# Optimization experiments

Measured on AMD Instinct MI355X. Metric: run time of the kernel, lower is better.

The kernel has to match this reference:

```python
import jax, jax.numpy as jnp
import numpy as np

D, K, RANK = 128, 64, 16

def setup_inputs() -> dict:
    key = jax.random.key(0)
    k1, k2, k3, k4, k5 = jax.random.split(key, 5)
    x1 = jax.random.normal(k1, (8, 16384, D), dtype=jnp.float32)
    x2 = jax.random.normal(k2, (8, 16384, D), dtype=jnp.float32)
    scale = (RANK * D) ** -0.5
    W_lin = jax.random.normal(k3, (K, D), dtype=jnp.float32) * (D ** -0.5)
    P = jax.random.normal(k4, (K, D, RANK), dtype=jnp.float32) * scale
    Q = jax.random.normal(k5, (K, D, RANK), dtype=jnp.float32) * scale
    return {"x1": x1, "x2": x2, "W_lin": W_lin, "P": P, "Q": Q}

def reference(x1, x2, W_lin, P, Q):
    z = x1 - x2                                   # (b,n,d)
    s = x1 + x2                                   # (b,n,d)
    lin = jnp.einsum('bnd,kd->bnk', z, W_lin)     # linear term (no bias)
    zP = jnp.einsum('bnd,kdr->bnkr', z, P)
    sQ = jnp.einsum('bnd,kdr->bnkr', s, Q)
    bili = jnp.sum(zP * sQ, axis=-1)              # (b,n,k)
    return lin + bili
```

## Files before the change

kernel.cpp:

```cpp
#include <hip/hip_runtime.h>
#include <hip/hip_bf16.h>

typedef short v8s __attribute__((ext_vector_type(8)));
typedef float v4f __attribute__((ext_vector_type(4)));

#define DD 128
#define KTOT 64
#define RANK 16

#define QOFF 131072
#define WOFF 262144

__device__ __forceinline__ unsigned int pk_bf16_trunc(float a, float b) {
  return __builtin_amdgcn_perm(__builtin_bit_cast(unsigned int, b),
                               __builtin_bit_cast(unsigned int, a),
                               0x07060302u);
}

__device__ __forceinline__ unsigned short bf16_rne(float x) {
  unsigned int u = __builtin_bit_cast(unsigned int, x);
  u += 0x7FFFu + ((u >> 16) & 1u);
  return (unsigned short)(u >> 16);
}

__global__ __launch_bounds__(256)
void swizzle_weights_kernel(const float* __restrict__ Wl,
                            const float* __restrict__ P,
                            const float* __restrict__ Q,
                            unsigned short* __restrict__ ws) {
  const int tid = blockIdx.x * 256 + threadIdx.x;
  if (tid < 16384) {
    const int kg   = tid >> 11;
    const int rr   = (tid >> 8) & 7;
    const int kk   = (tid >> 6) & 3;
    const int lane = tid & 63;
    const int q = lane >> 4, c = lane & 15;
    const int k = kg * 8 + (c & 7);
    const int r = rr * 2 + (c >> 3);
    const int dbase = (kk * 4 + q) * 8;
    const float* Pg = P + ((long)k * DD) * RANK + r;
    const float* Qg = Q + ((long)k * DD) * RANK + r;
    union { v8s v; unsigned short h[8]; } po, qo;
#pragma unroll
    for (int j = 0; j < 8; ++j) {
      po.h[j] = bf16_rne(Pg[(long)(dbase + j) * RANK]);
      qo.h[j] = bf16_rne(Qg[(long)(dbase + j) * RANK]);
    }
    *(v8s*)(ws + (long)tid * 8)        = po.v;
    *(v8s*)(ws + QOFF + (long)tid * 8) = qo.v;
  } else if (tid < 16384 + 2048) {
    const int t2   = tid - 16384;
    const int kg   = t2 >> 8;
    const int kk   = (t2 >> 6) & 3;
    const int lane = t2 & 63;
    const int q = lane >> 4, c = lane & 15;
    union { v8s v; unsigned short h[8]; } wo;
#pragma unroll
    for (int j = 0; j < 8; ++j) wo.h[j] = 0;
    if (c < 8) {
      const float* wrow = Wl + (long)(kg * 8 + c) * DD + (kk * 4 + q) * 8;
#pragma unroll
      for (int j = 0; j < 8; ++j) wo.h[j] = bf16_rne(wrow[j]);
    }
    *(v8s*)(ws + WOFF + (long)t2 * 8) = wo.v;
  }
}

__global__ __launch_bounds__(256, 2)
void antisym_bilinear_kernel(const float* __restrict__ x1,
                             const float* __restrict__ x2,
                             const unsigned short* __restrict__ wsw,
                             float* __restrict__ out) {
  const int b    = blockIdx.x;
  const int tid  = threadIdx.x;
  const int lane = tid & 63;
  const int wave = tid >> 6;
  const int q    = lane >> 4;
  const int c    = lane & 15;

  const int strip0 = b * 16 + wave * 4;

  v8s Zf[4][4], Sf[4][4];
#pragma unroll
  for (int t = 0; t < 4; ++t) {
    const int row = (strip0 + t) * 16 + c;
    const float4* p1 = (const float4*)(x1 + (long)row * DD);
    const float4* p2 = (const float4*)(x2 + (long)row * DD);
#pragma unroll
    for (int kk = 0; kk < 4; ++kk) {
      const int i0 = kk * 8 + q * 2;
      float4 a0 = p1[i0], a1 = p1[i0 + 1];
      float4 b0 = p2[i0], b1 = p2[i0 + 1];
      union { v8s v; unsigned int u[4]; } z, s;
      z.u[0] = pk_bf16_trunc(a0.x - b0.x, a0.y - b0.y);
      z.u[1] = pk_bf16_trunc(a0.z - b0.z, a0.w - b0.w);
      z.u[2] = pk_bf16_trunc(a1.x - b1.x, a1.y - b1.y);
      z.u[3] = pk_bf16_trunc(a1.z - b1.z, a1.w - b1.w);
      s.u[0] = pk_bf16_trunc(a0.x + b0.x, a0.y + b0.y);
      s.u[1] = pk_bf16_trunc(a0.z + b0.z, a0.w + b0.w);
      s.u[2] = pk_bf16_trunc(a1.x + b1.x, a1.y + b1.y);
      s.u[3] = pk_bf16_trunc(a1.z + b1.z, a1.w + b1.w);
      Zf[t][kk] = z.v;
      Sf[t][kk] = s.v;
    }
  }

  for (int kg = 0; kg < 8; ++kg) {
    v8s Wf[4];
#pragma unroll
    for (int kk = 0; kk < 4; ++kk)
      Wf[kk] = *(const v8s*)(wsw + WOFF + (((long)(kg * 4 + kk) * 64 + lane) * 8));

    v4f acc[4];
#pragma unroll
    for (int t = 0; t < 4; ++t) acc[t] = (v4f){0.f, 0.f, 0.f, 0.f};

#pragma unroll
    for (int rr = 0; rr < 8; ++rr) {
      v8s Pf[4], Qf[4];
#pragma unroll
      for (int kk = 0; kk < 4; ++kk) {
        const long off = (((long)((kg * 8 + rr) * 4 + kk) * 64 + lane)) * 8;
        Pf[kk] = *(const v8s*)(wsw + off);
        Qf[kk] = *(const v8s*)(wsw + QOFF + off);
      }
#pragma unroll
      for (int t = 0; t < 4; ++t) {
        v4f ap = (v4f){0.f, 0.f, 0.f, 0.f};
        v4f aq = (v4f){0.f, 0.f, 0.f, 0.f};
#pragma unroll
        for (int kk = 0; kk < 4; ++kk) {
          ap = __builtin_amdgcn_mfma_f32_16x16x32_bf16(Zf[t][kk], Pf[kk], ap, 0, 0, 0);
          aq = __builtin_amdgcn_mfma_f32_16x16x32_bf16(Sf[t][kk], Qf[kk], aq, 0, 0, 0);
        }
        acc[t] += ap * aq;
      }
    }

#pragma unroll
    for (int t = 0; t < 4; ++t) {
#pragma unroll
      for (int kk = 0; kk < 4; ++kk)
        acc[t] = __builtin_amdgcn_mfma_f32_16x16x32_bf16(Zf[t][kk], Wf[kk], acc[t], 0, 0, 0);
    }

#pragma unroll
    for (int t = 0; t < 4; ++t) {
      float v0 = acc[t][0], v1 = acc[t][1], v2 = acc[t][2], v3 = acc[t][3];
      v0 += __shfl_xor(v0, 8, 64);
      v1 += __shfl_xor(v1, 8, 64);
      v2 += __shfl_xor(v2, 8, 64);
      v3 += __shfl_xor(v3, 8, 64);
      const int row0 = (strip0 + t) * 16 + q * 4;
      const int cc = c & 7;
      float* op = out + (long)row0 * KTOT + kg * 8 + cc;
      if (c < 8) { op[0 * KTOT] = v0; op[1 * KTOT] = v1; }
      else       { op[2 * KTOT] = v2; op[3 * KTOT] = v3; }
    }
  }
}

extern "C" void kernel_launch(void* const* d_in, const int* in_sizes, int n_in,
                              void* d_out, int out_size, void* d_ws, size_t ws_size,
                              hipStream_t stream) {
  (void)in_sizes; (void)n_in; (void)ws_size; (void)out_size;
  const float* x1 = (const float*)d_in[0];
  const float* x2 = (const float*)d_in[1];
  const float* Wl = (const float*)d_in[2];
  const float* P  = (const float*)d_in[3];
  const float* Q  = (const float*)d_in[4];
  float* out = (float*)d_out;
  unsigned short* ws = (unsigned short*)d_ws;

  hipLaunchKernelGGL(swizzle_weights_kernel, dim3(72), dim3(256), 0, stream,
                     Wl, P, Q, ws);
  hipLaunchKernelGGL(antisym_bilinear_kernel, dim3(512), dim3(256), 0, stream,
                     x1, x2, ws, out);
}
```

Baseline: 216.6 us.

## Stage P/Q weight tiles in LDS with double-buffered async global-to-LDS loads

P and Q bf16 weight fragments are now copied into a double-buffered LDS area with global_load_lds, and each chunk is prefetched while the MFMA work runs on the previous one. Before, every wave read the same weight fragments straight from global memory on its own. The aim is to share one copy per block and hide load latency behind compute. In exchange the block uses 64KB of LDS, which may lower occupancy below the 2 blocks per CU set in launch bounds, and adds a barrier per half-group.

```diff
diff --git a/kernel.cpp b/kernel.cpp
--- a/kernel.cpp
+++ b/kernel.cpp
@@ -21,6 +21,13 @@
   unsigned int u = __builtin_bit_cast(unsigned int, x);
   u += 0x7FFFu + ((u >> 16) & 1u);
   return (unsigned short)(u >> 16);
+}
+
+__device__ __forceinline__ void gl_lds16(const unsigned short* g, unsigned short* l) {
+  __builtin_amdgcn_global_load_lds(
+      (const __attribute__((address_space(1))) void*)(uintptr_t)g,
+      (__attribute__((address_space(3))) void*)(uintptr_t)l,
+      16, 0, 0);
 }
 
 __global__ __launch_bounds__(256)
@@ -71,6 +78,8 @@
                              const float* __restrict__ x2,
                              const unsigned short* __restrict__ wsw,
                              float* __restrict__ out) {
+  __shared__ __align__(16) unsigned short lds[2][16384];
+
   const int b    = blockIdx.x;
   const int tid  = threadIdx.x;
   const int lane = tid & 63;
@@ -79,6 +88,18 @@
   const int c    = lane & 15;
 
   const int strip0 = b * 16 + wave * 4;
+
+  {
+    const unsigned short* gP = wsw;
+    const unsigned short* gQ = wsw + QOFF;
+    unsigned short* dP = &lds[0][0];
+#pragma unroll
+    for (int i = 0; i < 4; ++i) {
+      const int o = (i * 256 + tid) * 8;
+      gl_lds16(gP + o, dP + o);
+      gl_lds16(gQ + o, dP + 8192 + o);
+    }
+  }
 
   v8s Zf[4][4], Sf[4][4];
 #pragma unroll
@@ -105,6 +126,8 @@
     }
   }
 
+  __syncthreads();
+
   for (int kg = 0; kg < 8; ++kg) {
     v8s Wf[4];
 #pragma unroll
@@ -116,25 +139,46 @@
     for (int t = 0; t < 4; ++t) acc[t] = (v4f){0.f, 0.f, 0.f, 0.f};
 
 #pragma unroll
-    for (int rr = 0; rr < 8; ++rr) {
-      v8s Pf[4], Qf[4];
-#pragma unroll
-      for (int kk = 0; kk < 4; ++kk) {
-        const long off = (((long)((kg * 8 + rr) * 4 + kk) * 64 + lane)) * 8;
-        Pf[kk] = *(const v8s*)(wsw + off);
-        Qf[kk] = *(const v8s*)(wsw + QOFF + off);
+    for (int h = 0; h < 2; ++h) {
+      const int s = kg * 2 + h;
+
+      if (s < 15) {
+        const unsigned short* gP = wsw + (s + 1) * 8192;
+        const unsigned short* gQ = wsw + QOFF + (s + 1) * 8192;
+        unsigned short* dP = &lds[(s + 1) & 1][0];
+#pragma unroll
+        for (int i = 0; i < 4; ++i) {
+          const int o = (i * 256 + tid) * 8;
+          gl_lds16(gP + o, dP + o);
+          gl_lds16(gQ + o, dP + 8192 + o);
+        }
       }
-#pragma unroll
-      for (int t = 0; t < 4; ++t) {
-        v4f ap = (v4f){0.f, 0.f, 0.f, 0.f};
-        v4f aq = (v4f){0.f, 0.f, 0.f, 0.f};
+
+      const unsigned short* bP = &lds[s & 1][0];
+      const unsigned short* bQ = bP + 8192;
+
+#pragma unroll
+      for (int rl = 0; rl < 4; ++rl) {
+        v8s Pf[4], Qf[4];
 #pragma unroll
         for (int kk = 0; kk < 4; ++kk) {
-          ap = __builtin_amdgcn_mfma_f32_16x16x32_bf16(Zf[t][kk], Pf[kk], ap, 0, 0, 0);
-          aq = __builtin_amdgcn_mfma_f32_16x16x32_bf16(Sf[t][kk], Qf[kk], aq, 0, 0, 0);
+          const int off = ((rl * 4 + kk) * 64 + lane) * 8;
+          Pf[kk] = *(const v8s*)(bP + off);
+          Qf[kk] = *(const v8s*)(bQ + off);
         }
-        acc[t] += ap * aq;
+#pragma unroll
+        for (int t = 0; t < 4; ++t) {
+          v4f ap = (v4f){0.f, 0.f, 0.f, 0.f};
+          v4f aq = (v4f){0.f, 0.f, 0.f, 0.f};
+#pragma unroll
+          for (int kk = 0; kk < 4; ++kk) {
+            ap = __builtin_amdgcn_mfma_f32_16x16x32_bf16(Zf[t][kk], Pf[kk], ap, 0, 0, 0);
+            aq = __builtin_amdgcn_mfma_f32_16x16x32_bf16(Sf[t][kk], Qf[kk], aq, 0, 0, 0);
+          }
+          acc[t] += ap * aq;
+        }
       }
+      __syncthreads();
     }
 
 #pragma unroll
```

Measured after the change: 359.3 us. 1.66x slower.
